# Kernel optimization log

Measured on AMD Instinct MI355X. Metric: run time of the kernel, lower is better.

Reference implementation:

```python
import jax, jax.numpy as jnp
import numpy as np

N = 35          # nodes (hardcoded by x.repeat(35,1,1))
V = 4           # edge views
D1, D2, D3 = 512, 256, 128


def _full_graph_edges():
    # fully connected, no self loops, COO [2, E], E = 35*34
    src, dst = np.meshgrid(np.arange(N), np.arange(N), indexing='ij')
    mask = src != dst
    return np.stack([src[mask], dst[mask]], axis=0).astype(np.int64)


def setup_inputs() -> dict:
    key = jax.random.key(0)
    ks = jax.random.split(key, 8)
    E = N * (N - 1)
    edge_index = jnp.asarray(_full_graph_edges())
    s1, s2, s3 = 1.0 / np.sqrt(V), 1.0 / np.sqrt(V), 1.0 / np.sqrt(V)
    return {
        'x': jnp.ones((N, 1), jnp.float32),
        'edge_attr': jax.random.uniform(ks[0], (E, V), jnp.float32),
        'edge_index': edge_index,
        'mlp1_w': jax.random.normal(ks[1], (V, 1 * D1), jnp.float32) * s1,
        'mlp1_b': jnp.zeros((1 * D1,), jnp.float32),
        'root1': jax.random.normal(ks[2], (1, D1), jnp.float32),
        'bias1': jnp.zeros((D1,), jnp.float32),
        'mlp2_w': jax.random.normal(ks[3], (V, D1 * D2), jnp.float32) * s2,
        'mlp2_b': jnp.zeros((D1 * D2,), jnp.float32),
        'root2': jax.random.normal(ks[4], (D1, D2), jnp.float32) / np.sqrt(D1),
        'bias2': jnp.zeros((D2,), jnp.float32),
        'mlp3_w': jax.random.normal(ks[5], (V, D2 * D3), jnp.float32) * s3,
        'mlp3_b': jnp.zeros((D2 * D3,), jnp.float32),
        'root3': jax.random.normal(ks[6], (D2, D3), jnp.float32) / np.sqrt(D2),
        'bias3': jnp.zeros((D3,), jnp.float32),
    }


def _nnconv(x, edge_attr, src, dst, mlp_w, mlp_b, root, bias, in_c, out_c):
    # edge MLP -> per-edge weight matrix [E, in_c, out_c]
    w = jax.nn.relu(edge_attr @ mlp_w + mlp_b).reshape(-1, in_c, out_c)
    # gather source feats, per-edge matmul: [E, out_c]
    msg = jnp.einsum('ei,eio->eo', x[src], w)
    # scatter-mean to targets
    agg = jax.ops.segment_sum(msg, dst, num_segments=N)
    cnt = jax.ops.segment_sum(jnp.ones_like(msg[:, 0]), dst, num_segments=N)
    agg = agg / jnp.maximum(cnt, 1.0)[:, None]
    return agg + x @ root + bias


def reference(x, edge_attr, edge_index, mlp1_w, mlp1_b, root1, bias1,
              mlp2_w, mlp2_b, root2, bias2, mlp3_w, mlp3_b, root3, bias3):
    src, dst = edge_index[0], edge_index[1]
    h = jax.nn.relu(_nnconv(x, edge_attr, src, dst, mlp1_w, mlp1_b, root1, bias1, 1, D1))
    h = jax.nn.relu(_nnconv(h, edge_attr, src, dst, mlp2_w, mlp2_b, root2, bias2, D1, D2))
    h = jax.nn.relu(_nnconv(h, edge_attr, src, dst, mlp3_w, mlp3_b, root3, bias3, D2, D3))
    # cbt[a, i] = sum_f |h[i, f] - h[a, f]|   (repeat / transpose / abs / sum)
    cbt = jnp.sum(jnp.abs(h[None, :, :] - h[:, None, :]), axis=2)
    return cbt
```

## Files before the change

kernel.cpp:

```cpp
#include <hip/hip_runtime.h>

#define NN 35
#define NE 1190

__global__ __launch_bounds__(512)
void layer1_kernel(const float* __restrict__ x,
                   const float* __restrict__ ea,
                   const float* __restrict__ W1,
                   const float* __restrict__ b1,
                   const float* __restrict__ root1,
                   const float* __restrict__ bias1,
                   float* __restrict__ h1)
{
    const int d = blockIdx.x;
    const int o = threadIdx.x;
    const float w0 = W1[o], w1 = W1[512 + o], w2 = W1[1024 + o], w3 = W1[1536 + o];
    const float bb = b1[o];
    float sum = 0.f;
#pragma unroll
    for (int s = 0; s < NN; ++s) {
        if (s == d) continue;
        const int e = s * 34 + (d < s ? d : d - 1);
        const float4 a = ((const float4*)ea)[e];
        float w = fmaf(a.x, w0, fmaf(a.y, w1, fmaf(a.z, w2, fmaf(a.w, w3, bb))));
        sum = fmaf(x[s], fmaxf(w, 0.f), sum);
    }
    h1[d * 512 + o] = fmaxf(sum / 34.f + x[d] * root1[o] + bias1[o], 0.f);
}

template<int I, int O, int IC>
__global__ __launch_bounds__(O)
void edge_msg_acc(const float* __restrict__ h,
                  const float* __restrict__ ea,
                  const float* __restrict__ W,
                  const float* __restrict__ bias,
                  const float* __restrict__ root,
                  float* __restrict__ agg)
{
    constexpr int K4 = IC / 4;
    const int d  = blockIdx.x;
    const int c  = blockIdx.y;
    const int i0 = c * IC;
    const int o  = threadIdx.x;

    __shared__ __align__(16) float hs[35][IC];
    __shared__ float4 as[34];

    if (o < 35) {
        const int s = (o < 34) ? (o + (o >= d ? 1 : 0)) : d;
        const float4* hp = (const float4*)(h + (size_t)s * I + i0);
#pragma unroll
        for (int k = 0; k < K4; ++k) ((float4*)hs[o])[k] = hp[k];
    }
    if (o >= 64 && o < 98) {
        const int j = o - 64;
        const int s = j + (j >= d ? 1 : 0);
        as[j] = ((const float4*)ea)[s * 34 + (d < s ? d : d - 1)];
    }
    __syncthreads();

    float w0[IC], w1[IC], w2[IC], w3[IC], bb[IC], rr[IC];
#pragma unroll
    for (int i = 0; i < IC; ++i) {
        const size_t base = (size_t)(i0 + i) * O + o;
        w0[i] = W[0 * (size_t)I * O + base];
        w1[i] = W[1 * (size_t)I * O + base];
        w2[i] = W[2 * (size_t)I * O + base];
        w3[i] = W[3 * (size_t)I * O + base];
        bb[i] = bias[base];
        rr[i] = root[base];
    }

    float acc = 0.f;
#pragma unroll 2
    for (int j = 0; j < 34; ++j) {
        const float4 a = as[j];
#pragma unroll
        for (int k = 0; k < K4; ++k) {
            const float4 hv = ((const float4*)hs[j])[k];
            const float hm[4] = {hv.x, hv.y, hv.z, hv.w};
#pragma unroll
            for (int m = 0; m < 4; ++m) {
                const int i = k * 4 + m;
                float w = fmaf(a.x, w0[i], fmaf(a.y, w1[i],
                          fmaf(a.z, w2[i], fmaf(a.w, w3[i], bb[i]))));
                acc = fmaf(hm[m], fmaxf(w, 0.f), acc);
            }
        }
    }

    float racc = 0.f;
#pragma unroll
    for (int k = 0; k < K4; ++k) {
        const float4 hv = ((const float4*)hs[34])[k];
        const float hm[4] = {hv.x, hv.y, hv.z, hv.w};
#pragma unroll
        for (int m = 0; m < 4; ++m) racc = fmaf(hm[m], rr[k * 4 + m], racc);
    }

    atomicAdd(&agg[d * O + o], acc * (1.f / 34.f) + racc);
}

template<int O>
__global__ __launch_bounds__(O)
void act_kernel(const float* __restrict__ agg, const float* __restrict__ bias,
                float* __restrict__ hout)
{
    const int d = blockIdx.x;
    const int o = threadIdx.x;
    hout[d * O + o] = fmaxf(agg[d * O + o] + bias[o], 0.f);
}

__global__ void cbt_kernel(const float* __restrict__ h,
                           float* __restrict__ out)
{
    const int idx = blockIdx.x * blockDim.x + threadIdx.x;
    if (idx >= NN * NN) return;
    const int a = idx / NN;
    const int i = idx % NN;
    float sum = 0.f;
#pragma unroll 8
    for (int f = 0; f < 128; ++f)
        sum += fabsf(h[i * 128 + f] - h[a * 128 + f]);
    out[idx] = sum;
}

extern "C" void kernel_launch(void* const* d_in, const int* in_sizes, int n_in,
                              void* d_out, int out_size, void* d_ws, size_t ws_size,
                              hipStream_t stream) {
    const float* x       = (const float*)d_in[0];
    const float* ea      = (const float*)d_in[1];
    const float* mlp1_w  = (const float*)d_in[3];
    const float* mlp1_b  = (const float*)d_in[4];
    const float* root1   = (const float*)d_in[5];
    const float* bias1   = (const float*)d_in[6];
    const float* mlp2_w  = (const float*)d_in[7];
    const float* mlp2_b  = (const float*)d_in[8];
    const float* root2   = (const float*)d_in[9];
    const float* bias2   = (const float*)d_in[10];
    const float* mlp3_w  = (const float*)d_in[11];
    const float* mlp3_b  = (const float*)d_in[12];
    const float* root3   = (const float*)d_in[13];
    const float* bias3   = (const float*)d_in[14];
    float* out = (float*)d_out;

    float* ws   = (float*)d_ws;
    float* agg2 = ws;
    float* agg3 = agg2 + 35 * 256;
    float* h1   = agg3 + 35 * 128;
    float* h2   = h1 + 35 * 512;
    float* h3   = h2 + 35 * 256;

    hipMemsetAsync(ws, 0, (size_t)(35 * 256 + 35 * 128) * sizeof(float), stream);

    layer1_kernel<<<NN, 512, 0, stream>>>(x, ea, mlp1_w, mlp1_b, root1, bias1, h1);

    edge_msg_acc<512, 256, 16><<<dim3(NN, 32), 256, 0, stream>>>(h1, ea, mlp2_w, mlp2_b, root2, agg2);
    act_kernel<256><<<NN, 256, 0, stream>>>(agg2, bias2, h2);

    edge_msg_acc<256, 128, 8><<<dim3(NN, 32), 128, 0, stream>>>(h2, ea, mlp3_w, mlp3_b, root3, agg3);
    act_kernel<128><<<NN, 128, 0, stream>>>(agg3, bias3, h3);

    cbt_kernel<<<(NN * NN + 255) / 256, 256, 0, stream>>>(h3, out);
}
```

Before: 141.9 us.

## Fuse all layers into one cooperative persistent kernel with grid syncs

Replaces the memset plus six separate kernel launches with a single cooperative kernel of 256 blocks that uses grid-wide syncs between layer1, layer2, layer3 and the pairwise L1 distance stage. The activation passes are folded into the next stage's shared-memory load, and the distance stage uses one wavefront per output with a shuffle reduction. Layer 3 splits the edge loop across four thread groups so 512-thread blocks stay busy. The aim is to remove launch overhead and the intermediate round trips. In exchange each block runs several work units in sequence, pays for grid syncs, and the per-layer unit work is laid out differently from before. A non-cooperative fallback path is kept.

```diff
diff --git a/kernel.cpp b/kernel.cpp
--- a/kernel.cpp
+++ b/kernel.cpp
@@ -1,15 +1,208 @@
 #include <hip/hip_runtime.h>
+#include <hip/hip_cooperative_groups.h>
+
+namespace cg = cooperative_groups;
 
 #define NN 35
-#define NE 1190
+
 
 __global__ __launch_bounds__(512)
-void layer1_kernel(const float* __restrict__ x,
-                   const float* __restrict__ ea,
-                   const float* __restrict__ W1,
-                   const float* __restrict__ b1,
-                   const float* __restrict__ root1,
-                   const float* __restrict__ bias1,
+void mega_kernel(const float* __restrict__ x,
+                 const float* __restrict__ ea,
+                 const float* __restrict__ W1, const float* __restrict__ b1,
+                 const float* __restrict__ root1, const float* __restrict__ bias1,
+                 const float* __restrict__ W2, const float* __restrict__ b2,
+                 const float* __restrict__ root2, const float* __restrict__ bias2,
+                 const float* __restrict__ W3, const float* __restrict__ b3,
+                 const float* __restrict__ root3, const float* __restrict__ bias3,
+                 float* __restrict__ out,
+                 float* __restrict__ ws)
+{
+    cg::grid_group grid = cg::this_grid();
+    float* h1   = ws;
+    float* agg2 = h1 + 35 * 512;
+    float* agg3 = agg2 + 35 * 256;
+
+    const int b = blockIdx.x;
+    const int t = threadIdx.x;
+    const int gtid = b * 512 + t;
+
+    __shared__ __align__(16) float hs[35][16];
+    __shared__ __align__(16) float hs3[35][8];
+    __shared__ float4 as[34];
+
+    if (gtid < 35 * 256 + 35 * 128) agg2[gtid] = 0.f;
+    if (gtid < 35 * 512) {
+        const int d = gtid >> 9, o = gtid & 511;
+        const float u0 = W1[o], u1 = W1[512 + o], u2 = W1[1024 + o], u3 = W1[1536 + o];
+        const float bb = b1[o];
+        float sum = 0.f;
+#pragma unroll
+        for (int s = 0; s < NN; ++s) {
+            if (s == d) continue;
+            const float4 a = ((const float4*)ea)[s * 34 + (d < s ? d : d - 1)];
+            float w = fmaf(a.x, u0, fmaf(a.y, u1, fmaf(a.z, u2, fmaf(a.w, u3, bb))));
+            sum = fmaf(x[s], fmaxf(w, 0.f), sum);
+        }
+        h1[gtid] = fmaxf(sum * (1.f / 34.f) + x[d] * root1[o] + bias1[o], 0.f);
+    }
+    grid.sync();
+
+    for (int u = b; u < 35 * 32; u += 256) {
+        const int d  = u >> 5;
+        const int i0 = (u & 31) << 4;
+        if (t < 140) {
+            const int r = t >> 2, k = t & 3;
+            const int s = (r < 34) ? (r + (r >= d ? 1 : 0)) : d;
+            ((float4*)hs[r])[k] = ((const float4*)(h1 + s * 512 + i0))[k];
+        }
+        if (t >= 192 && t < 226) {
+            const int j = t - 192;
+            const int s = j + (j >= d ? 1 : 0);
+            as[j] = ((const float4*)ea)[s * 34 + (d < s ? d : d - 1)];
+        }
+        __syncthreads();
+
+        const int o = t & 255, half = t >> 8;
+        const int ib = half * 8;
+        float w0[8], w1r[8], w2r[8], w3r[8], bbr[8], rr[8];
+#pragma unroll
+        for (int i = 0; i < 8; ++i) {
+            const size_t base = (size_t)(i0 + ib + i) * 256 + o;
+            w0[i]  = W2[base];
+            w1r[i] = W2[131072 + base];
+            w2r[i] = W2[262144 + base];
+            w3r[i] = W2[393216 + base];
+            bbr[i] = b2[base];
+            rr[i]  = root2[base];
+        }
+        float acc0 = 0.f, acc1 = 0.f;
+        for (int j = 0; j < 34; ++j) {
+            const float4 a  = as[j];
+            const float4 h0 = ((const float4*)hs[j])[half * 2];
+            const float4 h1v = ((const float4*)hs[j])[half * 2 + 1];
+            const float hm[8] = {h0.x, h0.y, h0.z, h0.w, h1v.x, h1v.y, h1v.z, h1v.w};
+#pragma unroll
+            for (int i = 0; i < 4; ++i) {
+                float w = fmaf(a.x, w0[i], fmaf(a.y, w1r[i],
+                          fmaf(a.z, w2r[i], fmaf(a.w, w3r[i], bbr[i]))));
+                acc0 = fmaf(hm[i], fmaxf(w, 0.f), acc0);
+            }
+#pragma unroll
+            for (int i = 4; i < 8; ++i) {
+                float w = fmaf(a.x, w0[i], fmaf(a.y, w1r[i],
+                          fmaf(a.z, w2r[i], fmaf(a.w, w3r[i], bbr[i]))));
+                acc1 = fmaf(hm[i], fmaxf(w, 0.f), acc1);
+            }
+        }
+        const float4 r0 = ((const float4*)hs[34])[half * 2];
+        const float4 r1 = ((const float4*)hs[34])[half * 2 + 1];
+        const float rm[8] = {r0.x, r0.y, r0.z, r0.w, r1.x, r1.y, r1.z, r1.w};
+        float racc = 0.f;
+#pragma unroll
+        for (int i = 0; i < 8; ++i) racc = fmaf(rm[i], rr[i], racc);
+
+        atomicAdd(&agg2[d * 256 + o], (acc0 + acc1) * (1.f / 34.f) + racc);
+        __syncthreads();
+    }
+    grid.sync();
+
+    for (int u = b; u < 35 * 32; u += 256) {
+        const int d  = u >> 5;
+        const int i0 = (u & 31) << 3;
+        if (t < 70) {
+            const int r = t >> 1, k = t & 1;
+            const int s = (r < 34) ? (r + (r >= d ? 1 : 0)) : d;
+            float4 v  = ((const float4*)(agg2 + s * 256 + i0))[k];
+            const float4 bv = ((const float4*)(bias2 + i0))[k];
+            v.x = fmaxf(v.x + bv.x, 0.f);
+            v.y = fmaxf(v.y + bv.y, 0.f);
+            v.z = fmaxf(v.z + bv.z, 0.f);
+            v.w = fmaxf(v.w + bv.w, 0.f);
+            ((float4*)hs3[r])[k] = v;
+        }
+        if (t >= 128 && t < 162) {
+            const int j = t - 128;
+            const int s = j + (j >= d ? 1 : 0);
+            as[j] = ((const float4*)ea)[s * 34 + (d < s ? d : d - 1)];
+        }
+        __syncthreads();
+
+        const int o = t & 127, grp = t >> 7;
+        const int jstart = (grp < 2) ? grp * 9 : 18 + (grp - 2) * 8;
+        const int jcnt   = (grp < 2) ? 9 : 8;
+
+        float w0[8], w1r[8], w2r[8], w3r[8], bbr[8], rr[8];
+#pragma unroll
+        for (int i = 0; i < 8; ++i) {
+            const size_t base = (size_t)(i0 + i) * 128 + o;
+            w0[i]  = W3[base];
+            w1r[i] = W3[32768 + base];
+            w2r[i] = W3[65536 + base];
+            w3r[i] = W3[98304 + base];
+            bbr[i] = b3[base];
+            rr[i]  = root3[base];
+        }
+        float acc0 = 0.f, acc1 = 0.f;
+        for (int jj = 0; jj < jcnt; ++jj) {
+            const int j = jstart + jj;
+            const float4 a  = as[j];
+            const float4 h0 = ((const float4*)hs3[j])[0];
+            const float4 h1v = ((const float4*)hs3[j])[1];
+            const float hm[8] = {h0.x, h0.y, h0.z, h0.w, h1v.x, h1v.y, h1v.z, h1v.w};
+#pragma unroll
+            for (int i = 0; i < 4; ++i) {
+                float w = fmaf(a.x, w0[i], fmaf(a.y, w1r[i],
+                          fmaf(a.z, w2r[i], fmaf(a.w, w3r[i], bbr[i]))));
+                acc0 = fmaf(hm[i], fmaxf(w, 0.f), acc0);
+            }
+#pragma unroll
+            for (int i = 4; i < 8; ++i) {
+                float w = fmaf(a.x, w0[i], fmaf(a.y, w1r[i],
+                          fmaf(a.z, w2r[i], fmaf(a.w, w3r[i], bbr[i]))));
+                acc1 = fmaf(hm[i], fmaxf(w, 0.f), acc1);
+            }
+        }
+        float contrib = (acc0 + acc1) * (1.f / 34.f);
+        if (grp == 0) {
+            const float4 r0 = ((const float4*)hs3[34])[0];
+            const float4 r1 = ((const float4*)hs3[34])[1];
+            const float rm[8] = {r0.x, r0.y, r0.z, r0.w, r1.x, r1.y, r1.z, r1.w};
+            float racc = 0.f;
+#pragma unroll
+            for (int i = 0; i < 8; ++i) racc = fmaf(rm[i], rr[i], racc);
+            contrib += racc;
+        }
+        atomicAdd(&agg3[d * 128 + o], contrib);
+        __syncthreads();
+    }
+    grid.sync();
+
+    {
+        const int lane = t & 63;
+        for (int wv = b * 8 + (t >> 6); wv < NN * NN; wv += 256 * 8) {
+            const int a_ = wv / NN, i_ = wv % NN;
+            float s = 0.f;
+#pragma unroll
+            for (int q = 0; q < 2; ++q) {
+                const int f = lane + q * 64;
+                const float bb = bias3[f];
+                const float hi = fmaxf(agg3[i_ * 128 + f] + bb, 0.f);
+                const float ha = fmaxf(agg3[a_ * 128 + f] + bb, 0.f);
+                s += fabsf(hi - ha);
+            }
+#pragma unroll
+            for (int off = 32; off > 0; off >>= 1)
+                s += __shfl_xor(s, off, 64);
+            if (lane == 0) out[wv] = s;
+        }
+    }
+}
+
+__global__ __launch_bounds__(512)
+void layer1_kernel(const float* __restrict__ x, const float* __restrict__ ea,
+                   const float* __restrict__ W1, const float* __restrict__ b1,
+                   const float* __restrict__ root1, const float* __restrict__ bias1,
                    float* __restrict__ h1)
 {
     const int d = blockIdx.x;
@@ -20,8 +213,7 @@
 #pragma unroll
     for (int s = 0; s < NN; ++s) {
         if (s == d) continue;
-        const int e = s * 34 + (d < s ? d : d - 1);
-        const float4 a = ((const float4*)ea)[e];
+        const float4 a = ((const float4*)ea)[s * 34 + (d < s ? d : d - 1)];
         float w = fmaf(a.x, w0, fmaf(a.y, w1, fmaf(a.z, w2, fmaf(a.w, w3, bb))));
         sum = fmaf(x[s], fmaxf(w, 0.f), sum);
     }
@@ -30,12 +222,9 @@
 
 template<int I, int O, int IC>
 __global__ __launch_bounds__(O)
-void edge_msg_acc(const float* __restrict__ h,
-                  const float* __restrict__ ea,
-                  const float* __restrict__ W,
-                  const float* __restrict__ bias,
-                  const float* __restrict__ root,
-                  float* __restrict__ agg)
+void edge_msg_acc(const float* __restrict__ h, const float* __restrict__ ea,
+                  const float* __restrict__ W, const float* __restrict__ bias,
+                  const float* __restrict__ root, float* __restrict__ agg)
 {
     constexpr int K4 = IC / 4;
     const int d  = blockIdx.x;
@@ -70,7 +259,6 @@
         bb[i] = bias[base];
         rr[i] = root[base];
     }
-
     float acc = 0.f;
 #pragma unroll 2
     for (int j = 0; j < 34; ++j) {
@@ -88,7 +276,6 @@
             }
         }
     }
-
     float racc = 0.f;
 #pragma unroll
     for (int k = 0; k < K4; ++k) {
@@ -97,7 +284,6 @@
 #pragma unroll
         for (int m = 0; m < 4; ++m) racc = fmaf(hm[m], rr[k * 4 + m], racc);
     }
-
     atomicAdd(&agg[d * O + o], acc * (1.f / 34.f) + racc);
 }
 
@@ -106,13 +292,11 @@
 void act_kernel(const float* __restrict__ agg, const float* __restrict__ bias,
                 float* __restrict__ hout)
 {
-    const int d = blockIdx.x;
-    const int o = threadIdx.x;
-    hout[d * O + o] = fmaxf(agg[d * O + o] + bias[o], 0.f);
-}
-
-__global__ void cbt_kernel(const float* __restrict__ h,
-                           float* __restrict__ out)
+    hout[blockIdx.x * O + threadIdx.x] =
+        fmaxf(agg[blockIdx.x * O + threadIdx.x] + bias[threadIdx.x], 0.f);
+}
+
+__global__ void cbt_kernel(const float* __restrict__ h, float* __restrict__ out)
 {
     const int idx = blockIdx.x * blockDim.x + threadIdx.x;
     if (idx >= NN * NN) return;
@@ -128,38 +312,45 @@
 extern "C" void kernel_launch(void* const* d_in, const int* in_sizes, int n_in,
                               void* d_out, int out_size, void* d_ws, size_t ws_size,
                               hipStream_t stream) {
-    const float* x       = (const float*)d_in[0];
-    const float* ea      = (const float*)d_in[1];
-    const float* mlp1_w  = (const float*)d_in[3];
-    const float* mlp1_b  = (const float*)d_in[4];
-    const float* root1   = (const float*)d_in[5];
-    const float* bias1   = (const float*)d_in[6];
-    const float* mlp2_w  = (const float*)d_in[7];
-    const float* mlp2_b  = (const float*)d_in[8];
-    const float* root2   = (const float*)d_in[9];
-    const float* bias2   = (const float*)d_in[10];
-    const float* mlp3_w  = (const float*)d_in[11];
-    const float* mlp3_b  = (const float*)d_in[12];
-    const float* root3   = (const float*)d_in[13];
-    const float* bias3   = (const float*)d_in[14];
+    const float* x      = (const float*)d_in[0];
+    const float* ea     = (const float*)d_in[1];
+    const float* mlp1_w = (const float*)d_in[3];
+    const float* mlp1_b = (const float*)d_in[4];
+    const float* root1  = (const float*)d_in[5];
+    const float* bias1  = (const float*)d_in[6];
+    const float* mlp2_w = (const float*)d_in[7];
+    const float* mlp2_b = (const float*)d_in[8];
+    const float* root2  = (const float*)d_in[9];
+    const float* bias2  = (const float*)d_in[10];
+    const float* mlp3_w = (const float*)d_in[11];
+    const float* mlp3_b = (const float*)d_in[12];
+    const float* root3  = (const float*)d_in[13];
+    const float* bias3  = (const float*)d_in[14];
     float* out = (float*)d_out;
-
-    float* ws   = (float*)d_ws;
-    float* agg2 = ws;
+    float* ws  = (float*)d_ws;
+
+    float* h1   = ws;
+    float* agg2 = h1 + 35 * 512;
     float* agg3 = agg2 + 35 * 256;
-    float* h1   = agg3 + 35 * 128;
-    float* h2   = h1 + 35 * 512;
+    float* h2   = agg3 + 35 * 128;
     float* h3   = h2 + 35 * 256;
 
-    hipMemsetAsync(ws, 0, (size_t)(35 * 256 + 35 * 128) * sizeof(float), stream);
-
-    layer1_kernel<<<NN, 512, 0, stream>>>(x, ea, mlp1_w, mlp1_b, root1, bias1, h1);
-
-    edge_msg_acc<512, 256, 16><<<dim3(NN, 32), 256, 0, stream>>>(h1, ea, mlp2_w, mlp2_b, root2, agg2);
-    act_kernel<256><<<NN, 256, 0, stream>>>(agg2, bias2, h2);
-
-    edge_msg_acc<256, 128, 8><<<dim3(NN, 32), 128, 0, stream>>>(h2, ea, mlp3_w, mlp3_b, root3, agg3);
-    act_kernel<128><<<NN, 128, 0, stream>>>(agg3, bias3, h3);
-
-    cbt_kernel<<<(NN * NN + 255) / 256, 256, 0, stream>>>(h3, out);
-}
+    void* args[] = {
+        (void*)&x, (void*)&ea,
+        (void*)&mlp1_w, (void*)&mlp1_b, (void*)&root1, (void*)&bias1,
+        (void*)&mlp2_w, (void*)&mlp2_b, (void*)&root2, (void*)&bias2,
+        (void*)&mlp3_w, (void*)&mlp3_b, (void*)&root3, (void*)&bias3,
+        (void*)&out, (void*)&ws
+    };
+    hipError_t err = hipLaunchCooperativeKernel((void*)mega_kernel, dim3(256),
+                                                dim3(512), args, 0, stream);
+    if (err != hipSuccess) {
+        hipMemsetAsync(agg2, 0, (size_t)(35 * 256 + 35 * 128) * sizeof(float), stream);
+        layer1_kernel<<<NN, 512, 0, stream>>>(x, ea, mlp1_w, mlp1_b, root1, bias1, h1);
+        edge_msg_acc<512, 256, 16><<<dim3(NN, 32), 256, 0, stream>>>(h1, ea, mlp2_w, mlp2_b, root2, agg2);
+        act_kernel<256><<<NN, 256, 0, stream>>>(agg2, bias2, h2);
+        edge_msg_acc<256, 128, 8><<<dim3(NN, 32), 128, 0, stream>>>(h2, ea, mlp3_w, mlp3_b, root3, agg3);
+        act_kernel<128><<<NN, 128, 0, stream>>>(agg3, bias3, h3);
+        cbt_kernel<<<(NN * NN + 255) / 256, 256, 0, stream>>>(h3, out);
+    }
+}
```

After: 247.0 us. 1.74x slower.

## Fuse memset and activation kernels into neighbors, parallelize cbt reduction per wave

Applied to the files above, without the earlier changes.

Zeroing of the aggregation buffers moves into the layer-1 kernel, removing the separate memset. The bias+ReLU activation kernels are dropped: layer 3 applies bias2+ReLU while staging agg2 into shared memory, and the cbt kernel applies bias3+ReLU on the fly. The cbt kernel now uses one wavefront per output pair with a shuffle reduction instead of one thread looping over 128 features. Together this cuts the launch count from seven operations to four, trading a little redundant activation math for fewer launches and less serial work.

```diff
diff --git a/kernel.cpp b/kernel.cpp
--- a/kernel.cpp
+++ b/kernel.cpp
@@ -1,56 +1,55 @@
 #include <hip/hip_runtime.h>
 
 #define NN 35
-#define NE 1190
+
 
 __global__ __launch_bounds__(512)
 void layer1_kernel(const float* __restrict__ x,
                    const float* __restrict__ ea,
-                   const float* __restrict__ W1,
-                   const float* __restrict__ b1,
-                   const float* __restrict__ root1,
-                   const float* __restrict__ bias1,
-                   float* __restrict__ h1)
+                   const float* __restrict__ W1, const float* __restrict__ b1,
+                   const float* __restrict__ root1, const float* __restrict__ bias1,
+                   float* __restrict__ h1,
+                   float* __restrict__ aggz)
 {
     const int d = blockIdx.x;
     const int o = threadIdx.x;
+    const int gtid = d * 512 + o;
+    if (gtid < 35 * 384) aggz[gtid] = 0.f;
+
     const float w0 = W1[o], w1 = W1[512 + o], w2 = W1[1024 + o], w3 = W1[1536 + o];
     const float bb = b1[o];
     float sum = 0.f;
 #pragma unroll
     for (int s = 0; s < NN; ++s) {
         if (s == d) continue;
-        const int e = s * 34 + (d < s ? d : d - 1);
-        const float4 a = ((const float4*)ea)[e];
+        const float4 a = ((const float4*)ea)[s * 34 + (d < s ? d : d - 1)];
         float w = fmaf(a.x, w0, fmaf(a.y, w1, fmaf(a.z, w2, fmaf(a.w, w3, bb))));
         sum = fmaf(x[s], fmaxf(w, 0.f), sum);
     }
-    h1[d * 512 + o] = fmaxf(sum / 34.f + x[d] * root1[o] + bias1[o], 0.f);
-}
-
-template<int I, int O, int IC>
-__global__ __launch_bounds__(O)
-void edge_msg_acc(const float* __restrict__ h,
+    h1[gtid] = fmaxf(sum * (1.f / 34.f) + x[d] * root1[o] + bias1[o], 0.f);
+}
+
+__global__ __launch_bounds__(256, 2)
+void edge2_kernel(const float* __restrict__ h,
                   const float* __restrict__ ea,
                   const float* __restrict__ W,
                   const float* __restrict__ bias,
                   const float* __restrict__ root,
                   float* __restrict__ agg)
 {
-    constexpr int K4 = IC / 4;
     const int d  = blockIdx.x;
     const int c  = blockIdx.y;
-    const int i0 = c * IC;
+    const int i0 = c * 16;
     const int o  = threadIdx.x;
 
-    __shared__ __align__(16) float hs[35][IC];
+    __shared__ __align__(16) float hs[35][16];
     __shared__ float4 as[34];
 
     if (o < 35) {
         const int s = (o < 34) ? (o + (o >= d ? 1 : 0)) : d;
-        const float4* hp = (const float4*)(h + (size_t)s * I + i0);
-#pragma unroll
-        for (int k = 0; k < K4; ++k) ((float4*)hs[o])[k] = hp[k];
+        const float4* hp = (const float4*)(h + (size_t)s * 512 + i0);
+#pragma unroll
+        for (int k = 0; k < 4; ++k) ((float4*)hs[o])[k] = hp[k];
     }
     if (o >= 64 && o < 98) {
         const int j = o - 64;
@@ -59,24 +58,23 @@
     }
     __syncthreads();
 
-    float w0[IC], w1[IC], w2[IC], w3[IC], bb[IC], rr[IC];
-#pragma unroll
-    for (int i = 0; i < IC; ++i) {
-        const size_t base = (size_t)(i0 + i) * O + o;
-        w0[i] = W[0 * (size_t)I * O + base];
-        w1[i] = W[1 * (size_t)I * O + base];
-        w2[i] = W[2 * (size_t)I * O + base];
-        w3[i] = W[3 * (size_t)I * O + base];
+    float w0[16], w1[16], w2[16], w3[16], bb[16], rr[16];
+#pragma unroll
+    for (int i = 0; i < 16; ++i) {
+        const size_t base = (size_t)(i0 + i) * 256 + o;
+        w0[i] = W[base];
+        w1[i] = W[131072 + base];
+        w2[i] = W[262144 + base];
+        w3[i] = W[393216 + base];
         bb[i] = bias[base];
         rr[i] = root[base];
     }
-
     float acc = 0.f;
 #pragma unroll 2
     for (int j = 0; j < 34; ++j) {
         const float4 a = as[j];
 #pragma unroll
-        for (int k = 0; k < K4; ++k) {
+        for (int k = 0; k < 4; ++k) {
             const float4 hv = ((const float4*)hs[j])[k];
             const float hm[4] = {hv.x, hv.y, hv.z, hv.w};
 #pragma unroll
@@ -88,78 +86,141 @@
             }
         }
     }
-
     float racc = 0.f;
 #pragma unroll
-    for (int k = 0; k < K4; ++k) {
+    for (int k = 0; k < 4; ++k) {
         const float4 hv = ((const float4*)hs[34])[k];
         const float hm[4] = {hv.x, hv.y, hv.z, hv.w};
 #pragma unroll
         for (int m = 0; m < 4; ++m) racc = fmaf(hm[m], rr[k * 4 + m], racc);
     }
-
-    atomicAdd(&agg[d * O + o], acc * (1.f / 34.f) + racc);
-}
-
-template<int O>
-__global__ __launch_bounds__(O)
-void act_kernel(const float* __restrict__ agg, const float* __restrict__ bias,
-                float* __restrict__ hout)
-{
-    const int d = blockIdx.x;
-    const int o = threadIdx.x;
-    hout[d * O + o] = fmaxf(agg[d * O + o] + bias[o], 0.f);
-}
-
-__global__ void cbt_kernel(const float* __restrict__ h,
-                           float* __restrict__ out)
-{
-    const int idx = blockIdx.x * blockDim.x + threadIdx.x;
-    if (idx >= NN * NN) return;
-    const int a = idx / NN;
-    const int i = idx % NN;
-    float sum = 0.f;
-#pragma unroll 8
-    for (int f = 0; f < 128; ++f)
-        sum += fabsf(h[i * 128 + f] - h[a * 128 + f]);
-    out[idx] = sum;
+    atomicAdd(&agg[d * 256 + o], acc * (1.f / 34.f) + racc);
+}
+
+__global__ __launch_bounds__(128, 2)
+void edge3_kernel(const float* __restrict__ agg2,
+                  const float* __restrict__ bias2,
+                  const float* __restrict__ ea,
+                  const float* __restrict__ W,
+                  const float* __restrict__ bias,
+                  const float* __restrict__ root,
+                  float* __restrict__ agg)
+{
+    const int d  = blockIdx.x;
+    const int c  = blockIdx.y;
+    const int i0 = c * 8;
+    const int o  = threadIdx.x;
+
+    __shared__ __align__(16) float hs[35][8];
+    __shared__ float4 as[34];
+
+    if (o < 70) {
+        const int r = o >> 1, k = o & 1;
+        const int s = (r < 34) ? (r + (r >= d ? 1 : 0)) : d;
+        float4 v = ((const float4*)(agg2 + (size_t)s * 256 + i0))[k];
+        const float4 bv = ((const float4*)(bias2 + i0))[k];
+        v.x = fmaxf(v.x + bv.x, 0.f);
+        v.y = fmaxf(v.y + bv.y, 0.f);
+        v.z = fmaxf(v.z + bv.z, 0.f);
+        v.w = fmaxf(v.w + bv.w, 0.f);
+        ((float4*)hs[r])[k] = v;
+    }
+    if (o >= 94) {
+        const int j = o - 94;
+        const int s = j + (j >= d ? 1 : 0);
+        as[j] = ((const float4*)ea)[s * 34 + (d < s ? d : d - 1)];
+    }
+    __syncthreads();
+
+    float w0[8], w1[8], w2[8], w3[8], bb[8], rr[8];
+#pragma unroll
+    for (int i = 0; i < 8; ++i) {
+        const size_t base = (size_t)(i0 + i) * 128 + o;
+        w0[i] = W[base];
+        w1[i] = W[32768 + base];
+        w2[i] = W[65536 + base];
+        w3[i] = W[98304 + base];
+        bb[i] = bias[base];
+        rr[i] = root[base];
+    }
+    float acc = 0.f;
+#pragma unroll 2
+    for (int j = 0; j < 34; ++j) {
+        const float4 a = as[j];
+#pragma unroll
+        for (int k = 0; k < 2; ++k) {
+            const float4 hv = ((const float4*)hs[j])[k];
+            const float hm[4] = {hv.x, hv.y, hv.z, hv.w};
+#pragma unroll
+            for (int m = 0; m < 4; ++m) {
+                const int i = k * 4 + m;
+                float w = fmaf(a.x, w0[i], fmaf(a.y, w1[i],
+                          fmaf(a.z, w2[i], fmaf(a.w, w3[i], bb[i]))));
+                acc = fmaf(hm[m], fmaxf(w, 0.f), acc);
+            }
+        }
+    }
+    float racc = 0.f;
+#pragma unroll
+    for (int k = 0; k < 2; ++k) {
+        const float4 hv = ((const float4*)hs[34])[k];
+        const float hm[4] = {hv.x, hv.y, hv.z, hv.w};
+#pragma unroll
+        for (int m = 0; m < 4; ++m) racc = fmaf(hm[m], rr[k * 4 + m], racc);
+    }
+    atomicAdd(&agg[d * 128 + o], acc * (1.f / 34.f) + racc);
+}
+
+__global__ __launch_bounds__(256)
+void cbt_kernel(const float* __restrict__ agg3,
+                const float* __restrict__ bias3,
+                float* __restrict__ out)
+{
+    const int wv = blockIdx.x * 4 + (threadIdx.x >> 6);
+    const int lane = threadIdx.x & 63;
+    if (wv >= NN * NN) return;
+    const int a_ = wv / NN, i_ = wv % NN;
+    float s = 0.f;
+#pragma unroll
+    for (int q = 0; q < 2; ++q) {
+        const int f = lane + q * 64;
+        const float bb = bias3[f];
+        const float hi = fmaxf(agg3[i_ * 128 + f] + bb, 0.f);
+        const float ha = fmaxf(agg3[a_ * 128 + f] + bb, 0.f);
+        s += fabsf(hi - ha);
+    }
+#pragma unroll
+    for (int off = 32; off > 0; off >>= 1)
+        s += __shfl_xor(s, off, 64);
+    if (lane == 0) out[wv] = s;
 }
 
 extern "C" void kernel_launch(void* const* d_in, const int* in_sizes, int n_in,
                               void* d_out, int out_size, void* d_ws, size_t ws_size,
                               hipStream_t stream) {
-    const float* x       = (const float*)d_in[0];
-    const float* ea      = (const float*)d_in[1];
-    const float* mlp1_w  = (const float*)d_in[3];
-    const float* mlp1_b  = (const float*)d_in[4];
-    const float* root1   = (const float*)d_in[5];
-    const float* bias1   = (const float*)d_in[6];
-    const float* mlp2_w  = (const float*)d_in[7];
-    const float* mlp2_b  = (const float*)d_in[8];
-    const float* root2   = (const float*)d_in[9];
-    const float* bias2   = (const float*)d_in[10];
-    const float* mlp3_w  = (const float*)d_in[11];
-    const float* mlp3_b  = (const float*)d_in[12];
-    const float* root3   = (const float*)d_in[13];
-    const float* bias3   = (const float*)d_in[14];
+    const float* x      = (const float*)d_in[0];
+    const float* ea     = (const float*)d_in[1];
+    const float* mlp1_w = (const float*)d_in[3];
+    const float* mlp1_b = (const float*)d_in[4];
+    const float* root1  = (const float*)d_in[5];
+    const float* bias1  = (const float*)d_in[6];
+    const float* mlp2_w = (const float*)d_in[7];
+    const float* mlp2_b = (const float*)d_in[8];
+    const float* root2  = (const float*)d_in[9];
+    const float* bias2  = (const float*)d_in[10];
+    const float* mlp3_w = (const float*)d_in[11];
+    const float* mlp3_b = (const float*)d_in[12];
+    const float* root3  = (const float*)d_in[13];
+    const float* bias3  = (const float*)d_in[14];
     float* out = (float*)d_out;
 
     float* ws   = (float*)d_ws;
     float* agg2 = ws;
     float* agg3 = agg2 + 35 * 256;
     float* h1   = agg3 + 35 * 128;
-    float* h2   = h1 + 35 * 512;
-    float* h3   = h2 + 35 * 256;
-
-    hipMemsetAsync(ws, 0, (size_t)(35 * 256 + 35 * 128) * sizeof(float), stream);
-
-    layer1_kernel<<<NN, 512, 0, stream>>>(x, ea, mlp1_w, mlp1_b, root1, bias1, h1);
-
-    edge_msg_acc<512, 256, 16><<<dim3(NN, 32), 256, 0, stream>>>(h1, ea, mlp2_w, mlp2_b, root2, agg2);
-    act_kernel<256><<<NN, 256, 0, stream>>>(agg2, bias2, h2);
-
-    edge_msg_acc<256, 128, 8><<<dim3(NN, 32), 128, 0, stream>>>(h2, ea, mlp3_w, mlp3_b, root3, agg3);
-    act_kernel<128><<<NN, 128, 0, stream>>>(agg3, bias3, h3);
-
-    cbt_kernel<<<(NN * NN + 255) / 256, 256, 0, stream>>>(h3, out);
-}
+
+    layer1_kernel<<<NN, 512, 0, stream>>>(x, ea, mlp1_w, mlp1_b, root1, bias1, h1, agg2);
+    edge2_kernel<<<dim3(NN, 32), 256, 0, stream>>>(h1, ea, mlp2_w, mlp2_b, root2, agg2);
+    edge3_kernel<<<dim3(NN, 32), 128, 0, stream>>>(agg2, bias2, ea, mlp3_w, mlp3_b, root3, agg3);
+    cbt_kernel<<<(NN * NN + 3) / 4, 256, 0, stream>>>(agg3, bias3, out);
+}
```

Measured after the change: 132.3 us. -6.7%, faster.
